# Performance work log

Measured on AMD Instinct MI355X. Metric: run time of the kernel, lower is better.

Reference implementation:

```python
import jax, jax.numpy as jnp
import numpy as np

DT = 0.01
NUM_STEPS = 2
DIM = 8        # latentDim (q:4, p:4)
HID = 128      # hiddenDim
BATCH = 524288


def _hamiltonian(z, W1, b1, W2, b2, W3, b3):
    # MLP H: (batch, 8) -> (batch,) scalar energy, tanh activations
    h = jnp.tanh(z @ W1 + b1)
    h = jnp.tanh(h @ W2 + b2)
    return (h @ W3 + b3)[..., 0]


def _grad_h(z, W1, b1, W2, b2, W3, b3):
    # dH/dz, batched; mirrors torch.autograd.grad(H.sum(), z)
    # torch detaches z before grad (create_graph keeps param graph)
    zc = jax.lax.stop_gradient(z)
    return jax.grad(lambda zz: _hamiltonian(zz, W1, b1, W2, b2, W3, b3).sum())(zc)


def setup_inputs() -> dict:
    key = jax.random.key(0)
    ks = jax.random.split(key, 7)
    z = jax.random.normal(ks[0], (BATCH, DIM), dtype=jnp.float32)
    W1 = jax.random.normal(ks[1], (DIM, HID), dtype=jnp.float32) / np.float32(np.sqrt(DIM))
    b1 = jnp.zeros((HID,), dtype=jnp.float32)
    W2 = jax.random.normal(ks[2], (HID, HID), dtype=jnp.float32) / np.float32(np.sqrt(HID))
    b2 = jnp.zeros((HID,), dtype=jnp.float32)
    W3 = jax.random.normal(ks[3], (HID, 1), dtype=jnp.float32) / np.float32(np.sqrt(HID))
    b3 = jnp.zeros((1,), dtype=jnp.float32)
    return {"z": z, "W1": W1, "b1": b1, "W2": W2, "b2": b2, "W3": W3, "b3": b3}


def reference(z, W1, b1, W2, b2, W3, b3):
    q, p = jnp.split(z, 2, axis=1)
    for _ in range(NUM_STEPS):
        g = _grad_h(jnp.concatenate([q, p], axis=1), W1, b1, W2, b2, W3, b3)
        dHdq, dHdp = jnp.split(g, 2, axis=1)
        p_half = p - 0.5 * DT * dHdq
        q_new = q + DT * dHdp
        g2 = _grad_h(jnp.concatenate([q_new, p_half], axis=1), W1, b1, W2, b2, W3, b3)
        dHdq_new = jnp.split(g2, 2, axis=1)[0]
        p = p_half - 0.5 * DT * dHdq_new
        q = q_new
    return jnp.concatenate([q, p], axis=1)
```

## Files before the change

kernel.cpp:

```cpp
#include <hip/hip_runtime.h>


typedef float f32x2 __attribute__((ext_vector_type(2)));
typedef float f32x4 __attribute__((ext_vector_type(4)));
typedef int   i32x2 __attribute__((ext_vector_type(2)));
typedef int   i32x4 __attribute__((ext_vector_type(4)));
typedef int   i32x8 __attribute__((ext_vector_type(8)));

#define DT 0.01f
#define S1 64.0f
#define TWO_LOG2E 2.8853900817779268f
#define SCL1 0x7F7F7F7F

#define OFF_W1B 0
#define OFF_W2B 1024
#define OFF_W2T 17408
#define OFF_W1T 33792
#define WTOT    34816

__device__ __forceinline__ unsigned char to_fp8(float x) {
    return (unsigned char)(__builtin_amdgcn_cvt_pk_fp8_f32(x, x, 0, false) & 0xff);
}
__device__ __forceinline__ float fexp2(float x) {
#if __has_builtin(__builtin_amdgcn_exp2f)
    return __builtin_amdgcn_exp2f(x);
#else
    return exp2f(x);
#endif
}
__device__ __forceinline__ float frcp(float x) {
#if __has_builtin(__builtin_amdgcn_rcpf)
    return __builtin_amdgcn_rcpf(x);
#else
    return 1.0f / x;
#endif
}

__device__ __forceinline__ i32x2 tr8(unsigned char* p) {
#if __has_builtin(__builtin_amdgcn_ds_read_tr8_b64)
    return __builtin_amdgcn_ds_read_tr8_b64((__attribute__((address_space(3))) i32x2*)p);
#else
    i32x2 d;
    asm volatile("ds_read_b64_tr_b8 %0, %1\n\ts_waitcnt lgkmcnt(0)"
                 : "=v"(d)
                 : "v"((unsigned)(unsigned long long)(__attribute__((address_space(3))) void*)p)
                 : "memory");
    __builtin_amdgcn_sched_barrier(0);
    return d;
#endif
}

__device__ __forceinline__ i32x8 cat44(i32x4 a, i32x4 b) {
    return __builtin_shufflevector(a, b, 0, 1, 2, 3, 4, 5, 6, 7);
}

__device__ __forceinline__ i32x8 read_a(unsigned char* abase) {
    i32x2 a0 = tr8(abase);
    i32x2 a1 = tr8(abase + 512);
    i32x2 a2 = tr8(abase + 1024);
    i32x2 a3 = tr8(abase + 1536);
    i32x4 lo = __builtin_shufflevector(a0, a1, 0, 1, 2, 3);
    i32x4 hi = __builtin_shufflevector(a2, a3, 0, 1, 2, 3);
    return cat44(lo, hi);
}

__device__ __forceinline__ f32x4 mm128(i32x8 a, i32x8 b, f32x4 c) {
#if __has_builtin(__builtin_amdgcn_mfma_scale_f32_16x16x128_f8f6f4)
    return __builtin_amdgcn_mfma_scale_f32_16x16x128_f8f6f4(a, b, c, 0, 0, 0, SCL1, 0, SCL1);
#else
    #pragma unroll
    for (int kt = 0; kt < 4; kt++) {
        long long aa = ((long long)(unsigned)a[2 * kt + 1] << 32) | (unsigned)a[2 * kt];
        long long bb = ((long long)(unsigned)b[2 * kt + 1] << 32) | (unsigned)b[2 * kt];
        c = __builtin_amdgcn_mfma_f32_16x16x32_fp8_fp8(aa, bb, c, 0, 0, 0);
    }
    return c;
#endif
}

#define NWAVES 7

__global__ __launch_bounds__(64 * NWAVES) void hnn_leapfrog_kernel(
    const float* __restrict__ Z, const float* __restrict__ W1,
    const float* __restrict__ B1f, const float* __restrict__ W2,
    const float* __restrict__ B2f, const float* __restrict__ W3,
    float* __restrict__ OUT, int njobs)
{
    __shared__ __align__(16) unsigned char sWT[WTOT];
    __shared__ __align__(16) unsigned char sACT[NWAVES * 2048];
    __shared__ __align__(16) float sZ[NWAVES * 128];

    const int t = threadIdx.x;

    for (int i = t; i < 1024; i += 64 * NWAVES) {
        int row = i >> 7, col = i & 127;
        float w = W1[i];
        sWT[OFF_W1B + (col >> 4) * 128 + (col & 15) * 8 + row] = to_fp8(w * TWO_LOG2E);
        int c = col >> 5, h = c >> 1, s = (c & 1) * 8 + (col & 7);
        int qd2 = (col >> 3) & 3;
        sWT[OFF_W1T + ((h * 4 + qd2) * 8 + row) * 16 + s] = to_fp8(w);
    }
    for (int i = t; i < 16384; i += 64 * NWAVES) {
        int row = i >> 7, col = i & 127;
        float w = W2[i];
        {
            int c = row >> 5, h = c >> 1, s = (c & 1) * 8 + (row & 7);
            int qd2 = (row >> 3) & 3;
            sWT[OFF_W2B + (((col >> 4) * 2 + h) * 64 + qd2 * 16 + (col & 15)) * 16 + s] =
                to_fp8(w * TWO_LOG2E);
        }
        {
            int c = col >> 5, h = c >> 1, s = (c & 1) * 8 + (col & 7);
            int qd2 = (col >> 3) & 3;
            sWT[OFF_W2T + (((row >> 4) * 2 + h) * 64 + qd2 * 16 + (row & 15)) * 16 + s] =
                to_fp8(w * 256.0f * W3[col]);
        }
    }

    const int lane = t & 63;
    const int wv   = t >> 6;
    const int nn   = lane & 15;
    const int qd   = lane >> 4;

    float eb1v[8], eb2v[8];
    #pragma unroll
    for (int nt = 0; nt < 8; nt++) {
        eb1v[nt] = fexp2(B1f[nt * 16 + nn] * TWO_LOG2E);
        eb2v[nt] = fexp2(B2f[nt * 16 + nn] * TWO_LOG2E);
    }
    __syncthreads();

    unsigned char* act   = sACT + wv * 2048;
    float*         zrow  = sZ + wv * 128;
    unsigned char* abase = act + qd * 128 + nn;
    unsigned char* awr   = act + nn * 16 + qd * 4;
    const unsigned char* w1b  = sWT + OFF_W1B + nn * 8;
    const unsigned char* w16  = sWT + lane * 16;
    const unsigned char* w1t  = sWT + OFF_W1T + (qd * 8 + (nn & 7)) * 16;

    const f32x4 zc = {0.f, 0.f, 0.f, 0.f};
    const int stride = gridDim.x * NWAVES;

    #pragma unroll 1
    for (int job = blockIdx.x * NWAVES + wv; job < njobs; job += stride) {
        f32x2 zv = ((const f32x2*)(Z + job * 128))[lane];
        ((f32x2*)zrow)[lane] = zv;

        #pragma unroll 1
        for (int ev = 0; ev < 4; ev++) {
            long long az = 0;
            if (qd == 0) {
                const f32x4* zr = (const f32x4*)(zrow + nn * 8);
                f32x4 z0 = zr[0], z1 = zr[1];
                int lo = __builtin_amdgcn_cvt_pk_fp8_f32(z0[0], z0[1], 0, false);
                lo     = __builtin_amdgcn_cvt_pk_fp8_f32(z0[2], z0[3], lo, true);
                int hi = __builtin_amdgcn_cvt_pk_fp8_f32(z1[0], z1[1], 0, false);
                hi     = __builtin_amdgcn_cvt_pk_fp8_f32(z1[2], z1[3], hi, true);
                az = ((long long)(unsigned)hi << 32) | (unsigned)lo;
            }
            float hc[8][4];
            #pragma unroll
            for (int nt = 0; nt < 8; nt++) {
                long long bf = *(const long long*)(w1b + nt * 128);
                f32x4 c = __builtin_amdgcn_mfma_f32_16x16x32_fp8_fp8(az, bf, zc, 0, 0, 0);
                #pragma unroll
                for (int r = 0; r < 4; r++) {
                    float e  = fexp2(c[r]);
                    float rr = frcp(fmaf(e, eb1v[nt], 1.0f));
                    hc[nt][r] = fmaf(-2.0f, rr, 1.0f);
                }
                int v = __builtin_amdgcn_cvt_pk_fp8_f32(hc[nt][0], hc[nt][1], 0, false);
                v     = __builtin_amdgcn_cvt_pk_fp8_f32(hc[nt][2], hc[nt][3], v, true);
                *(int*)(awr + nt * 256) = v;
            }
            i32x8 a8 = read_a(abase);
            #pragma unroll
            for (int nt = 0; nt < 8; nt++) {
                i32x4 bA = *(const i32x4*)(w16 + OFF_W2B + nt * 2048);
                i32x4 bB = *(const i32x4*)(w16 + OFF_W2B + nt * 2048 + 1024);
                f32x4 c = mm128(a8, cat44(bA, bB), zc);
                float dd[4];
                #pragma unroll
                for (int r = 0; r < 4; r++) {
                    float e  = fexp2(c[r]);
                    float rr = frcp(fmaf(e, eb2v[nt], 1.0f));
                    dd[r] = fmaf(-rr, rr, rr);
                }
                int v = __builtin_amdgcn_cvt_pk_fp8_f32(dd[0], dd[1], 0, false);
                v     = __builtin_amdgcn_cvt_pk_fp8_f32(dd[2], dd[3], v, true);
                *(int*)(awr + nt * 256) = v;
            }
            a8 = read_a(abase);
            #pragma unroll
            for (int nt = 0; nt < 8; nt++) {
                i32x4 bA = *(const i32x4*)(w16 + OFF_W2T + nt * 2048);
                i32x4 bB = *(const i32x4*)(w16 + OFF_W2T + nt * 2048 + 1024);
                f32x4 c = mm128(a8, cat44(bA, bB), zc);
                float dd[4];
                #pragma unroll
                for (int r = 0; r < 4; r++) {
                    float h = hc[nt][r];
                    dd[r] = c[r] * fmaf(-h, h, 1.0f);
                }
                int v = __builtin_amdgcn_cvt_pk_fp8_f32(dd[0], dd[1], 0, false);
                v     = __builtin_amdgcn_cvt_pk_fp8_f32(dd[2], dd[3], v, true);
                *(int*)(awr + nt * 256) = v;
            }
            a8 = read_a(abase);
            i32x4 bA = *(const i32x4*)(w1t);
            i32x4 bB = *(const i32x4*)(w1t + 512);
            f32x4 g = mm128(a8, cat44(bA, bB), zc);
            const bool first = (ev & 1) == 0;
            if (nn < 4) {
                float* p = zrow + qd * 32 + nn + 4;
                #pragma unroll
                for (int r = 0; r < 4; r++) p[r * 8] -= (0.5f * DT / S1) * g[r];
            } else if (nn < 8 && first) {
                float* p = zrow + qd * 32 + (nn - 4);
                #pragma unroll
                for (int r = 0; r < 4; r++) p[r * 8] += (DT / S1) * g[r];
            }
        }

        OUT[job * 128 + lane]      = zrow[lane];
        OUT[job * 128 + 64 + lane] = zrow[64 + lane];
    }
}

extern "C" void kernel_launch(void* const* d_in, const int* in_sizes, int n_in,
                              void* d_out, int out_size, void* d_ws, size_t ws_size,
                              hipStream_t stream) {
    const float* Z  = (const float*)d_in[0];
    const float* W1 = (const float*)d_in[1];
    const float* B1 = (const float*)d_in[2];
    const float* W2 = (const float*)d_in[3];
    const float* B2 = (const float*)d_in[4];
    const float* W3 = (const float*)d_in[5];
    float* OUT = (float*)d_out;
    int njobs = in_sizes[0] / 128;
    int grid  = 256 * 3;
    int maxg  = (njobs + NWAVES - 1) / NWAVES;
    if (grid > maxg) grid = maxg;
    hipLaunchKernelGGL(hnn_leapfrog_kernel, dim3(grid), dim3(64 * NWAVES), 0, stream,
                       Z, W1, B1, W2, B2, W3, OUT, njobs);
}
```

Measured before the change: 285.1 us.

## Use atomic work-stealing job queue with Z prefetch and vectorized W2 staging

Replaces the static grid-stride job loop with a per-wave atomic counter that hands out the next job dynamically, and prefetches the next job's Z rows before computing the current one. Weight staging of W2 now loads float4 vectors instead of scalars, and waves per block drop from 7 to 6. The goal is better load balance across waves and hiding global-load latency. In exchange it adds an atomic per job, a memset before each launch, and a workspace dependency.

Result: slower. 481.0 us (+68.7%).

```diff
diff --git a/kernel.cpp b/kernel.cpp
--- a/kernel.cpp
+++ b/kernel.cpp
@@ -78,13 +78,14 @@
 #endif
 }
 
-#define NWAVES 7
-
-__global__ __launch_bounds__(64 * NWAVES) void hnn_leapfrog_kernel(
+#define NWAVES 6
+#define BLOCKT (64 * NWAVES)
+
+__global__ __launch_bounds__(BLOCKT) void hnn_leapfrog_kernel(
     const float* __restrict__ Z, const float* __restrict__ W1,
     const float* __restrict__ B1f, const float* __restrict__ W2,
     const float* __restrict__ B2f, const float* __restrict__ W3,
-    float* __restrict__ OUT, int njobs)
+    float* __restrict__ OUT, int* __restrict__ cnt, int njobs, int nslots)
 {
     __shared__ __align__(16) unsigned char sWT[WTOT];
     __shared__ __align__(16) unsigned char sACT[NWAVES * 2048];
@@ -92,7 +93,7 @@
 
     const int t = threadIdx.x;
 
-    for (int i = t; i < 1024; i += 64 * NWAVES) {
+    for (int i = t; i < 1024; i += BLOCKT) {
         int row = i >> 7, col = i & 127;
         float w = W1[i];
         sWT[OFF_W1B + (col >> 4) * 128 + (col & 15) * 8 + row] = to_fp8(w * TWO_LOG2E);
@@ -100,20 +101,21 @@
         int qd2 = (col >> 3) & 3;
         sWT[OFF_W1T + ((h * 4 + qd2) * 8 + row) * 16 + s] = to_fp8(w);
     }
-    for (int i = t; i < 16384; i += 64 * NWAVES) {
-        int row = i >> 7, col = i & 127;
-        float w = W2[i];
-        {
-            int c = row >> 5, h = c >> 1, s = (c & 1) * 8 + (row & 7);
-            int qd2 = (row >> 3) & 3;
-            sWT[OFF_W2B + (((col >> 4) * 2 + h) * 64 + qd2 * 16 + (col & 15)) * 16 + s] =
-                to_fp8(w * TWO_LOG2E);
-        }
-        {
-            int c = col >> 5, h = c >> 1, s = (c & 1) * 8 + (col & 7);
-            int qd2 = (col >> 3) & 3;
-            sWT[OFF_W2T + (((row >> 4) * 2 + h) * 64 + qd2 * 16 + (row & 15)) * 16 + s] =
-                to_fp8(w * 256.0f * W3[col]);
+    for (int i = t; i < 4096; i += BLOCKT) {
+        f32x4 w = ((const f32x4*)W2)[i];
+        int base = i * 4;
+        int row = base >> 7, col0 = base & 127;
+        int cR = row >> 5, hR = cR >> 1, sR = (cR & 1) * 8 + (row & 7);
+        int qR = (row >> 3) & 3;
+        #pragma unroll
+        for (int u = 0; u < 4; u++) {
+            int col = col0 + u;
+            sWT[OFF_W2B + (((col >> 4) * 2 + hR) * 64 + qR * 16 + (col & 15)) * 16 + sR] =
+                to_fp8(w[u] * TWO_LOG2E);
+            int cC = col >> 5, hC = cC >> 1, sC = (cC & 1) * 8 + (col & 7);
+            int qC = (col >> 3) & 3;
+            sWT[OFF_W2T + (((row >> 4) * 2 + hC) * 64 + qC * 16 + (row & 15)) * 16 + sC] =
+                to_fp8(w[u] * 256.0f * W3[col]);
         }
     }
 
@@ -139,11 +141,20 @@
     const unsigned char* w1t  = sWT + OFF_W1T + (qd * 8 + (nn & 7)) * 16;
 
     const f32x4 zc = {0.f, 0.f, 0.f, 0.f};
-    const int stride = gridDim.x * NWAVES;
+
+    int job = blockIdx.x * NWAVES + wv;
+    int jcl = job < njobs ? job : 0;
+    f32x2 zv = ((const f32x2*)(Z + jcl * 128))[lane];
 
     #pragma unroll 1
-    for (int job = blockIdx.x * NWAVES + wv; job < njobs; job += stride) {
-        f32x2 zv = ((const f32x2*)(Z + job * 128))[lane];
+    while (job < njobs) {
+        int tk = 0;
+        if (lane == 0) tk = atomicAdd(cnt, 1);
+        tk = __builtin_amdgcn_readfirstlane(tk);
+        int nxt = nslots + tk;
+        int ncl = nxt < njobs ? nxt : 0;
+        f32x2 zn = ((const f32x2*)(Z + ncl * 128))[lane];
+
         ((f32x2*)zrow)[lane] = zv;
 
         #pragma unroll 1
@@ -224,6 +235,9 @@
 
         OUT[job * 128 + lane]      = zrow[lane];
         OUT[job * 128 + 64 + lane] = zrow[64 + lane];
+
+        job = nxt;
+        zv  = zn;
     }
 }
 
@@ -241,6 +255,8 @@
     int grid  = 256 * 3;
     int maxg  = (njobs + NWAVES - 1) / NWAVES;
     if (grid > maxg) grid = maxg;
-    hipLaunchKernelGGL(hnn_leapfrog_kernel, dim3(grid), dim3(64 * NWAVES), 0, stream,
-                       Z, W1, B1, W2, B2, W3, OUT, njobs);
-}
+    int nslots = grid * NWAVES;
+    hipMemsetAsync(d_ws, 0, 4, stream);
+    hipLaunchKernelGGL(hnn_leapfrog_kernel, dim3(grid), dim3(BLOCKT), 0, stream,
+                       Z, W1, B1, W2, B2, W3, OUT, (int*)d_ws, njobs, nslots);
+}
```
